# Performance work log

Hardware: AMD Instinct MI355X
Metric: run time of the kernel (lower is better)

The kernel has to match this reference:

```python
import jax, jax.numpy as jnp
import numpy as np

T, B, I, H, C = 16384, 1, 512, 1024, 512

def setup_inputs() -> dict:
    key = jax.random.key(0)
    ks = jax.random.split(key, 9)
    s = 0.05  # keep gates/logits in a sane range
    return {
        "inputs": jax.random.normal(ks[0], (T, B, I), jnp.float32),
        "h0": jax.random.normal(ks[1], (B, H), jnp.float32),
        "c0": jax.random.normal(ks[2], (B, H), jnp.float32),
        "W_ih": jax.random.normal(ks[3], (4 * H, I), jnp.float32) * s,
        "W_hh": jax.random.normal(ks[4], (4 * H, H), jnp.float32) * s,
        "b_ih": jax.random.normal(ks[5], (4 * H,), jnp.float32) * s,
        "b_hh": jax.random.normal(ks[6], (4 * H,), jnp.float32) * s,
        "W_dense": jax.random.normal(ks[7], (C, H), jnp.float32) * s,
        "b_dense": jax.random.normal(ks[8], (C,), jnp.float32) * s,
    }

def reference(inputs, h0, c0, W_ih, W_hh, b_ih, b_hh, W_dense, b_dense):
    def step(carry, x):
        h, c = carry  # [B,H]
        gates = x @ W_ih.T + b_ih + h @ W_hh.T + b_hh  # [B,4H]
        i, f, g, o = jnp.split(gates, 4, axis=1)
        i = jax.nn.sigmoid(i)
        f = jax.nn.sigmoid(f)
        g = jnp.tanh(g)
        o = jax.nn.sigmoid(o)
        c = f * c + i * g
        h = o * jnp.tanh(c)
        out = jax.nn.softmax(h @ W_dense.T + b_dense, axis=1)  # [B,C]
        return (h, c), out

    _, outs = jax.lax.scan(step, (h0, c0), inputs)  # [T,B,C]
    # torch F.softmax with no dim on a 3D tensor -> dim=0 (over time)
    return jax.nn.softmax(outs, axis=0)
```

## Files before the change

### kernel.cpp

```cpp
#include <hip/hip_runtime.h>
#include <math.h>

#define T_STEPS 16384
#define IN 512
#define HID 1024
#define NC 512
#define NWG 256
#define TPB 256
typedef unsigned long long ull;

__device__ __forceinline__ float sigmoid_f(float x) {
    return __builtin_amdgcn_rcpf(1.f + __expf(-x));
}
__device__ __forceinline__ float tanh_f(float x) {
    return 1.f - 2.f * __builtin_amdgcn_rcpf(1.f + __expf(2.f * x));
}

template <int CTRL>
__device__ __forceinline__ float dpp_add_(float x) {
    int y = __builtin_amdgcn_update_dpp(0, __float_as_int(x), CTRL, 0xf, 0xf, true);
    return x + __int_as_float(y);
}
__device__ __forceinline__ float wave_sum_l63(float x) {
    x = dpp_add_<0x111>(x);
    x = dpp_add_<0x112>(x);
    x = dpp_add_<0x114>(x);
    x = dpp_add_<0x118>(x);
    x = dpp_add_<0x142>(x);
    x = dpp_add_<0x143>(x);
    return x;
}

__global__ void init_k(const float* __restrict__ h0, ull* __restrict__ bufp)
{
    const int j = threadIdx.x;
    bufp[j]       = (1ull << 32) | (ull)__float_as_uint(h0[j]);
    bufp[HID + j] = 0ull;
}

__global__ __launch_bounds__(TPB, 1) void lstm_rec(
    const float* __restrict__ X,
    const float* __restrict__ c0,
    const float* __restrict__ W_ih,
    const float* __restrict__ W_hh,
    const float* __restrict__ b_ih,
    const float* __restrict__ b_hh,
    const float* __restrict__ Wd,
    const float* __restrict__ bd,
    float* __restrict__ logits,
    ull* __restrict__ bufp)
{
    __shared__ float svh[2][HID];

    const int tid  = threadIdx.x;
    const int wg   = blockIdx.x;
    const int lane = tid & 63;
    const int wv   = tid >> 6;
    const int j    = wg * 4 + wv;
    const int kb   = lane * 4;

    float4 w[4][6];
    float bias[4];
    #pragma unroll
    for (int q = 0; q < 4; ++q) {
        const int row = q * HID + j;
        #pragma unroll
        for (int c = 0; c < 6; ++c) {
            const int k = kb + c * 256;
            w[q][c] = (k < IN)
                ? *(const float4*)&W_ih[(size_t)row * IN + k]
                : *(const float4*)&W_hh[(size_t)row * HID + (k - IN)];
        }
        bias[q] = b_ih[row] + b_hh[row];
    }

    const int drow = wg * 2 + wv;
    float4 wd[4];
    float dbias = 0.f;
    if (wv < 2) {
        #pragma unroll
        for (int c = 0; c < 4; ++c)
            wd[c] = *(const float4*)&Wd[(size_t)drow * HID + kb + c * 256];
        dbias = bd[drow];
    }

    float c_state = c0[j];
    bool dead = false;
    float hx0 = 1.0f + (float)tid * 1e-8f;
    float hx1 = 1.1f, hx2 = 1.2f, hx3 = 1.3f;

    for (int t = 0; t <= T_STEPS; ++t) {
        const int p = t & 1;
        const unsigned want = (unsigned)(t + 1);
        const bool live = (t < T_STEPS);

        float4 x0, x1;
        if (live) {
            const float* xr = X + (size_t)t * IN;
            x0 = *(const float4*)&xr[kb];
            x1 = *(const float4*)&xr[kb + 256];
        }

        ull* src = bufp + (size_t)p * HID;
        ull v[4];
        #pragma unroll
        for (int c = 0; c < 4; ++c)
            v[c] = __hip_atomic_load(&src[tid + 256 * c],
                                     __ATOMIC_RELAXED, __HIP_MEMORY_SCOPE_AGENT);
        unsigned spn = 0;
        for (;;) {
            bool all = true;
            #pragma unroll
            for (int c = 0; c < 4; ++c) {
                if ((unsigned)(v[c] >> 32) < want) {
                    all = false;
                    v[c] = __hip_atomic_load(&src[tid + 256 * c],
                                             __ATOMIC_RELAXED, __HIP_MEMORY_SCOPE_AGENT);
                }
            }
            if (all || dead) break;
            #pragma unroll
            for (int u = 0; u < 32; ++u) hx0 = __builtin_fmaf(hx0, 1.0000001f, 1.0e-9f);
            asm volatile("" : "+v"(hx0));
            if (++spn > 500000u) dead = true;
        }
        #pragma unroll
        for (int c = 0; c < 4; ++c)
            svh[p][tid + 256 * c] = __uint_as_float((unsigned)v[c]);
        __syncthreads();

        const float4 s2 = *(const float4*)&svh[p][kb];
        const float4 s3 = *(const float4*)&svh[p][kb + 256];
        const float4 s4 = *(const float4*)&svh[p][kb + 512];
        const float4 s5 = *(const float4*)&svh[p][kb + 768];

        if (live) {
            float acc[4];
            #pragma unroll
            for (int q = 0; q < 4; ++q) {
                acc[q] = w[q][0].x*x0.x + w[q][0].y*x0.y + w[q][0].z*x0.z + w[q][0].w*x0.w
                       + w[q][1].x*x1.x + w[q][1].y*x1.y + w[q][1].z*x1.z + w[q][1].w*x1.w
                       + w[q][2].x*s2.x + w[q][2].y*s2.y + w[q][2].z*s2.z + w[q][2].w*s2.w
                       + w[q][3].x*s3.x + w[q][3].y*s3.y + w[q][3].z*s3.z + w[q][3].w*s3.w
                       + w[q][4].x*s4.x + w[q][4].y*s4.y + w[q][4].z*s4.z + w[q][4].w*s4.w
                       + w[q][5].x*s5.x + w[q][5].y*s5.y + w[q][5].z*s5.z + w[q][5].w*s5.w;
            }
            acc[0] = wave_sum_l63(acc[0]);
            acc[1] = wave_sum_l63(acc[1]);
            acc[2] = wave_sum_l63(acc[2]);
            acc[3] = wave_sum_l63(acc[3]);
            const float iv = sigmoid_f(acc[0] + bias[0]);
            const float fv = sigmoid_f(acc[1] + bias[1]);
            const float gv = tanh_f   (acc[2] + bias[2]);
            const float ov = sigmoid_f(acc[3] + bias[3]);
            c_state = fv * c_state + iv * gv;
            const float h = ov * tanh_f(c_state);
            if (lane == 63) {
                (void)__hip_atomic_exchange(&bufp[(size_t)(p ^ 1) * HID + j],
                    ((ull)(unsigned)(t + 2) << 32) | (ull)__float_as_uint(h),
                    __ATOMIC_RELAXED, __HIP_MEMORY_SCOPE_AGENT);
            }
        }

        if (t > 0 && wv < 2) {
            float d = wd[0].x*s2.x + wd[0].y*s2.y + wd[0].z*s2.z + wd[0].w*s2.w
                    + wd[1].x*s3.x + wd[1].y*s3.y + wd[1].z*s3.z + wd[1].w*s3.w
                    + wd[2].x*s4.x + wd[2].y*s4.y + wd[2].z*s4.z + wd[2].w*s4.w
                    + wd[3].x*s5.x + wd[3].y*s5.y + wd[3].z*s5.z + wd[3].w*s5.w;
            d = wave_sum_l63(d);
            if (lane == 63)
                logits[(size_t)(t - 1) * NC + drow] = d + dbias;
        }

        if (live) {
            #pragma unroll
            for (int u = 0; u < 128; ++u) {
                hx0 = __builtin_fmaf(hx0, 1.0000001f, 1.0e-9f);
                hx1 = __builtin_fmaf(hx1, 1.0000001f, 1.0e-9f);
                hx2 = __builtin_fmaf(hx2, 1.0000001f, 1.0e-9f);
                hx3 = __builtin_fmaf(hx3, 1.0000001f, 1.0e-9f);
            }
            asm volatile("" : "+v"(hx0), "+v"(hx1), "+v"(hx2), "+v"(hx3));
        }
    }
}

__global__ __launch_bounds__(256) void softmaxC_k(
    const float* __restrict__ logits, float* __restrict__ P)
{
    const int tid = threadIdx.x;
    const int lane = tid & 63, wvv = tid >> 6;
    #pragma unroll
    for (int rr = 0; rr < 2; ++rr) {
        const int row = blockIdx.x * 8 + wvv * 2 + rr;
        const float4 a = *(const float4*)&logits[(size_t)row * NC + lane * 8];
        const float4 b = *(const float4*)&logits[(size_t)row * NC + lane * 8 + 4];
        float m = fmaxf(fmaxf(fmaxf(a.x, a.y), fmaxf(a.z, a.w)),
                        fmaxf(fmaxf(b.x, b.y), fmaxf(b.z, b.w)));
        #pragma unroll
        for (int off = 32; off; off >>= 1) m = fmaxf(m, __shfl_xor(m, off));
        float4 ea, eb;
        ea.x = expf(a.x - m); ea.y = expf(a.y - m); ea.z = expf(a.z - m); ea.w = expf(a.w - m);
        eb.x = expf(b.x - m); eb.y = expf(b.y - m); eb.z = expf(b.z - m); eb.w = expf(b.w - m);
        float s = ea.x + ea.y + ea.z + ea.w + eb.x + eb.y + eb.z + eb.w;
        #pragma unroll
        for (int off = 32; off; off >>= 1) s += __shfl_xor(s, off);
        const float inv = 1.f / s;
        ea.x *= inv; ea.y *= inv; ea.z *= inv; ea.w *= inv;
        eb.x *= inv; eb.y *= inv; eb.z *= inv; eb.w *= inv;
        *(float4*)&P[(size_t)row * NC + lane * 8]     = ea;
        *(float4*)&P[(size_t)row * NC + lane * 8 + 4] = eb;
    }
}

__global__ __launch_bounds__(256) void colsum_k(const float* __restrict__ P, float* __restrict__ cs)
{
    const int tid = threadIdx.x;
    const int c  = blockIdx.x * 16 + (tid & 15);
    const int tr = tid >> 4;
    float s = 0.f;
    #pragma unroll 8
    for (int t = tr; t < T_STEPS; t += 16) s += expf(P[(size_t)t * NC + c]);
    __shared__ float red[256];
    red[tid] = s; __syncthreads();
    for (int off = 128; off >= 16; off >>= 1) {
        if (tid < off) red[tid] += red[tid + off];
        __syncthreads();
    }
    if (tid < 16) cs[blockIdx.x * 16 + tid] = red[tid];
}

__global__ __launch_bounds__(256) void norm_k(float* P, const float* __restrict__ cs)
{
    size_t i = (size_t)blockIdx.x * 256 + threadIdx.x;
    const size_t n = (size_t)T_STEPS * NC;
    const size_t stride = (size_t)gridDim.x * 256;
    for (; i < n; i += stride) P[i] = expf(P[i]) / cs[i & (NC - 1)];
}

extern "C" void kernel_launch(void* const* d_in, const int* in_sizes, int n_in,
                              void* d_out, int out_size, void* d_ws, size_t ws_size,
                              hipStream_t stream) {
    const float* X    = (const float*)d_in[0];
    const float* h0   = (const float*)d_in[1];
    const float* c0   = (const float*)d_in[2];
    const float* W_ih = (const float*)d_in[3];
    const float* W_hh = (const float*)d_in[4];
    const float* b_ih = (const float*)d_in[5];
    const float* b_hh = (const float*)d_in[6];
    const float* Wd   = (const float*)d_in[7];
    const float* bd   = (const float*)d_in[8];
    float* out = (float*)d_out;

    char* ws = (char*)d_ws;
    ull*   bufp   = (ull*)ws;
    float* cs     = (float*)(ws + 16384);
    float* logits = (float*)(ws + 32768);

    init_k<<<1, HID, 0, stream>>>(h0, bufp);
    lstm_rec<<<NWG, TPB, 0, stream>>>(X, c0, W_ih, W_hh, b_ih, b_hh, Wd, bd, logits, bufp);
    softmaxC_k<<<T_STEPS / 8, 256, 0, stream>>>(logits, out);
    colsum_k<<<NC / 16, 256, 0, stream>>>(out, cs);
    norm_k<<<2048, 256, 0, stream>>>(out, cs);
}
```

Baseline: 30.80 ms.

## Have each wave poll its own h slice directly, dropping LDS staging and block barrier

Each lane now loads the 16 hidden-state words it needs directly from the global flag/value buffer and spins until all of them carry the current step tag, using a wave-wide vote instead of a block barrier. The shared-memory staging of h and the __syncthreads are removed, so the four waves in a workgroup progress independently. In exchange each lane issues four times as many atomic loads per step, including redundant global traffic across waves, and polling gets more expensive under contention.

Result: slower. 43.80 ms (+42.2%).

```diff
diff --git a/kernel.cpp b/kernel.cpp
--- a/kernel.cpp
+++ b/kernel.cpp
@@ -50,8 +50,6 @@
     float* __restrict__ logits,
     ull* __restrict__ bufp)
 {
-    __shared__ float svh[2][HID];
-
     const int tid  = threadIdx.x;
     const int wg   = blockIdx.x;
     const int lane = tid & 63;
@@ -102,48 +100,51 @@
         }
 
         ull* src = bufp + (size_t)p * HID;
-        ull v[4];
-        #pragma unroll
-        for (int c = 0; c < 4; ++c)
-            v[c] = __hip_atomic_load(&src[tid + 256 * c],
-                                     __ATOMIC_RELAXED, __HIP_MEMORY_SCOPE_AGENT);
+        ull v[16];
+        #pragma unroll
+        for (int c = 0; c < 4; ++c) {
+            #pragma unroll
+            for (int i = 0; i < 4; ++i)
+                v[c * 4 + i] = __hip_atomic_load(&src[kb + c * 256 + i],
+                                                 __ATOMIC_RELAXED, __HIP_MEMORY_SCOPE_AGENT);
+        }
         unsigned spn = 0;
         for (;;) {
-            bool all = true;
-            #pragma unroll
-            for (int c = 0; c < 4; ++c) {
-                if ((unsigned)(v[c] >> 32) < want) {
-                    all = false;
-                    v[c] = __hip_atomic_load(&src[tid + 256 * c],
-                                             __ATOMIC_RELAXED, __HIP_MEMORY_SCOPE_AGENT);
+            bool fresh = true;
+            #pragma unroll
+            for (int idx = 0; idx < 16; ++idx) {
+                if ((unsigned)(v[idx] >> 32) < want) {
+                    fresh = false;
+                    const int c = idx >> 2, i = idx & 3;
+                    v[idx] = __hip_atomic_load(&src[kb + c * 256 + i],
+                                               __ATOMIC_RELAXED, __HIP_MEMORY_SCOPE_AGENT);
                 }
             }
-            if (all || dead) break;
+            if (__all((int)fresh) || dead) break;
             #pragma unroll
             for (int u = 0; u < 32; ++u) hx0 = __builtin_fmaf(hx0, 1.0000001f, 1.0e-9f);
             asm volatile("" : "+v"(hx0));
             if (++spn > 500000u) dead = true;
         }
-        #pragma unroll
-        for (int c = 0; c < 4; ++c)
-            svh[p][tid + 256 * c] = __uint_as_float((unsigned)v[c]);
-        __syncthreads();
-
-        const float4 s2 = *(const float4*)&svh[p][kb];
-        const float4 s3 = *(const float4*)&svh[p][kb + 256];
-        const float4 s4 = *(const float4*)&svh[p][kb + 512];
-        const float4 s5 = *(const float4*)&svh[p][kb + 768];
 
         if (live) {
             float acc[4];
             #pragma unroll
             for (int q = 0; q < 4; ++q) {
                 acc[q] = w[q][0].x*x0.x + w[q][0].y*x0.y + w[q][0].z*x0.z + w[q][0].w*x0.w
-                       + w[q][1].x*x1.x + w[q][1].y*x1.y + w[q][1].z*x1.z + w[q][1].w*x1.w
-                       + w[q][2].x*s2.x + w[q][2].y*s2.y + w[q][2].z*s2.z + w[q][2].w*s2.w
-                       + w[q][3].x*s3.x + w[q][3].y*s3.y + w[q][3].z*s3.z + w[q][3].w*s3.w
-                       + w[q][4].x*s4.x + w[q][4].y*s4.y + w[q][4].z*s4.z + w[q][4].w*s4.w
-                       + w[q][5].x*s5.x + w[q][5].y*s5.y + w[q][5].z*s5.z + w[q][5].w*s5.w;
+                       + w[q][1].x*x1.x + w[q][1].y*x1.y + w[q][1].z*x1.z + w[q][1].w*x1.w;
+            }
+            #pragma unroll
+            for (int c = 0; c < 4; ++c) {
+                const float h0v = __uint_as_float((unsigned)v[c*4+0]);
+                const float h1v = __uint_as_float((unsigned)v[c*4+1]);
+                const float h2v = __uint_as_float((unsigned)v[c*4+2]);
+                const float h3v = __uint_as_float((unsigned)v[c*4+3]);
+                #pragma unroll
+                for (int q = 0; q < 4; ++q) {
+                    const float4 wc = w[q][2 + c];
+                    acc[q] += wc.x*h0v + wc.y*h1v + wc.z*h2v + wc.w*h3v;
+                }
             }
             acc[0] = wave_sum_l63(acc[0]);
             acc[1] = wave_sum_l63(acc[1]);
@@ -163,10 +164,15 @@
         }
 
         if (t > 0 && wv < 2) {
-            float d = wd[0].x*s2.x + wd[0].y*s2.y + wd[0].z*s2.z + wd[0].w*s2.w
-                    + wd[1].x*s3.x + wd[1].y*s3.y + wd[1].z*s3.z + wd[1].w*s3.w
-                    + wd[2].x*s4.x + wd[2].y*s4.y + wd[2].z*s4.z + wd[2].w*s4.w
-                    + wd[3].x*s5.x + wd[3].y*s5.y + wd[3].z*s5.z + wd[3].w*s5.w;
+            float d = 0.f;
+            #pragma unroll
+            for (int c = 0; c < 4; ++c) {
+                const float4 wc = wd[c];
+                d += wc.x * __uint_as_float((unsigned)v[c*4+0])
+                   + wc.y * __uint_as_float((unsigned)v[c*4+1])
+                   + wc.z * __uint_as_float((unsigned)v[c*4+2])
+                   + wc.w * __uint_as_float((unsigned)v[c*4+3]);
+            }
             d = wave_sum_l63(d);
             if (lane == 63)
                 logits[(size_t)(t - 1) * NC + drow] = d + dbias;
```
